# Optimization experiments

Hardware: AMD Instinct MI355X
Metric: run time of the kernel (lower is better)

The kernel has to match this reference:

```python
import jax, jax.numpy as jnp
import numpy as np

LN_EPS = 1e-5

def layer_norm(x, w, b):
    mu = jnp.mean(x, axis=-1, keepdims=True)
    var = jnp.mean(jnp.square(x - mu), axis=-1, keepdims=True)
    return (x - mu) * jax.lax.rsqrt(var + LN_EPS) * w + b

def adaptive_mask_np(aa, bb, ada_para=0.2):
    # True = disallowed (matches torch ~bool mask). Static shapes -> numpy.
    adaptive_num = int(bb * ada_para)
    cc = bb // aa
    i = np.arange(aa)
    start = i * cc
    end = start + cc + adaptive_num
    over = end > bb - 1
    start = np.where(over, np.maximum(start - (end - (bb - 1)), 0), start)
    end = np.where(over, bb, end)
    cols = np.arange(bb)
    allowed = (cols[None, :] >= start[:, None]) & (cols[None, :] < end[:, None])
    return jnp.asarray(~allowed)  # [aa, bb] bool

def setup_inputs() -> dict:
    key = jax.random.key(0)
    ks = jax.random.split(key, 20)
    Lq, Lk, B, d, dff = 512, 4096, 4, 512, 2048
    s = lambda k, shape: jax.random.normal(k, shape, dtype=jnp.float32) * 0.02
    inp = {
        'tgt': jax.random.normal(ks[0], (Lq, B, d), dtype=jnp.float32),
        'memory': jax.random.normal(ks[1], (Lk, B, d), dtype=jnp.float32),
        'Wq': s(ks[2], (d, d)), 'bq': jnp.zeros((d,), jnp.float32),
        'Wk': s(ks[3], (d, d)), 'bk': jnp.zeros((d,), jnp.float32),
        'Wv': s(ks[4], (d, d)), 'bv': jnp.zeros((d,), jnp.float32),
        'Wo': s(ks[5], (d, d)), 'bo': jnp.zeros((d,), jnp.float32),
        'W1': s(ks[6], (dff, d)), 'b1': jnp.zeros((dff,), jnp.float32),
        'W2': s(ks[7], (d, dff)), 'b2': jnp.zeros((d,), jnp.float32),
        'ln1_w': jnp.ones((d,), jnp.float32), 'ln1_b': jnp.zeros((d,), jnp.float32),
        'ln2_w': jnp.ones((d,), jnp.float32), 'ln2_b': jnp.zeros((d,), jnp.float32),
        'ln3_w': jnp.ones((d,), jnp.float32), 'ln3_b': jnp.zeros((d,), jnp.float32),
        'ln4_w': jnp.ones((d,), jnp.float32), 'ln4_b': jnp.zeros((d,), jnp.float32),
    }
    return inp

def reference(tgt, memory, Wq, bq, Wk, bk, Wv, bv, Wo, bo, W1, b1, W2, b2,
              ln1_w, ln1_b, ln2_w, ln2_b, ln3_w, ln3_b, ln4_w, ln4_b):
    Lq, B, d = tgt.shape
    Lk = memory.shape[0]
    H = 8
    hd = d // H
    scale = 1.0 / jnp.sqrt(jnp.asarray(hd, tgt.dtype))

    t = layer_norm(tgt, ln1_w, ln1_b)      # [Lq,B,d]
    m = layer_norm(memory, ln2_w, ln2_b)   # [Lk,B,d]

    mask = adaptive_mask_np(Lq, Lk, 0.2)   # [Lq,Lk] bool, True=masked

    q = (t @ Wq.T + bq).reshape(Lq, B, H, hd)
    k = (m @ Wk.T + bk).reshape(Lk, B, H, hd)
    v = (m @ Wv.T + bv).reshape(Lk, B, H, hd)

    scores = jnp.einsum('qbhd,kbhd->bhqk', q * scale, k)
    scores = jnp.where(mask[None, None], -jnp.inf, scores)
    p = jax.nn.softmax(scores, axis=-1)                   # [B,H,Lq,Lk]
    attn_weights = jnp.mean(p, axis=1)                    # [B,Lq,Lk] (avg over heads)

    ctx = jnp.einsum('bhqk,kbhd->qbhd', p, v).reshape(Lq, B, d)
    tgt2 = ctx @ Wo.T + bo

    x = t + tgt2                       # dropout1 = identity (eval)
    x = layer_norm(x, ln3_w, ln3_b)
    ff = jax.nn.relu(x @ W1.T + b1) @ W2.T + b2
    x = x + ff                         # dropout2 = identity (eval)
    x = layer_norm(x, ln4_w, ln4_b)
    return (x, attn_weights)
```

## Files before the change

### kernel.cpp

```cpp
#include <hip/hip_runtime.h>
#include <hip/hip_bf16.h>

typedef __hip_bfloat16 bf16_t;
typedef __bf16 bf16x8 __attribute__((ext_vector_type(8)));
typedef float f32x4 __attribute__((ext_vector_type(4)));

#define LQ 512
#define LK 4096
#define BATCH 4
#define DMODEL 512
#define NHEAD 8
#define HEADDIM 64
#define DFF 2048
#define LN_EPS 1e-5f

__device__ inline float tofl(float x) { return x; }
__device__ inline float tofl(bf16_t x) { return __bfloat162float(x); }
__device__ inline void stfl(float* p, float v) { *p = v; }
__device__ inline void stfl(bf16_t* p, float v) { *p = __float2bfloat16(v); }

__device__ __forceinline__ void gld_lds16(const bf16_t* g, void* lds_base) {
    __builtin_amdgcn_global_load_lds(
        (const __attribute__((address_space(1))) uint32_t*)g,
        (__attribute__((address_space(3))) uint32_t*)lds_base, 16, 0, 0);
}

__global__ void prep_kernel(const float* __restrict__ s0, const float* __restrict__ s1,
                            const float* __restrict__ s2, const float* __restrict__ s3,
                            const float* __restrict__ s4, const float* __restrict__ s5,
                            bf16_t* __restrict__ wqkvo, bf16_t* __restrict__ w1bf,
                            bf16_t* __restrict__ w2bf, float* __restrict__ zbuf) {
    int bid = blockIdx.x;
    int tid = threadIdx.x;
    if (bid < 3072) {
        int t = bid * 256 + tid;
        int which = t >> 16;
        int idx = (t & 65535) * 4;
        const float* s; bf16_t* d;
        if (which < 4) {
            s = (which == 0 ? s0 : which == 1 ? s1 : which == 2 ? s2 : s3) ;
            d = wqkvo + (size_t)which * 262144;
        } else if (which < 8) {
            s = s4 + (size_t)(which - 4) * 262144;
            d = w1bf + (size_t)(which - 4) * 262144;
        } else {
            s = s5 + (size_t)(which - 8) * 262144;
            d = w2bf + (size_t)(which - 8) * 262144;
        }
        float4 v = *(const float4*)(s + idx);
        d[idx + 0] = __float2bfloat16(v.x);
        d[idx + 1] = __float2bfloat16(v.y);
        d[idx + 2] = __float2bfloat16(v.z);
        d[idx + 3] = __float2bfloat16(v.w);
    } else {
        size_t i = ((size_t)(bid - 3072) * 256 + tid) * 4;
        float4 z = {0.f, 0.f, 0.f, 0.f};
        *(float4*)(zbuf + i) = z;
    }
}

template <typename TOUT, bool DUAL>
__global__ void ln_kernel(const float* __restrict__ in, const float* __restrict__ w,
                          const float* __restrict__ b, TOUT* __restrict__ out1,
                          float* __restrict__ out2) {
    __shared__ float red[256];
    const int row = blockIdx.x;
    const int tid = threadIdx.x;
    const float* x = in + (size_t)row * DMODEL;
    float v0 = x[tid];
    float v1 = x[tid + 256];

    red[tid] = v0 + v1;
    __syncthreads();
    for (int s = 128; s > 0; s >>= 1) { if (tid < s) red[tid] += red[tid + s]; __syncthreads(); }
    float mu = red[0] * (1.0f / DMODEL);
    __syncthreads();

    float d0 = v0 - mu, d1 = v1 - mu;
    red[tid] = d0 * d0 + d1 * d1;
    __syncthreads();
    for (int s = 128; s > 0; s >>= 1) { if (tid < s) red[tid] += red[tid + s]; __syncthreads(); }
    float inv = rsqrtf(red[0] * (1.0f / DMODEL) + LN_EPS);

    float r0 = d0 * inv * w[tid] + b[tid];
    float r1 = d1 * inv * w[tid + 256] + b[tid + 256];
    TOUT* o = out1 + (size_t)row * DMODEL;
    stfl(&o[tid], r0);
    stfl(&o[tid + 256], r1);
    if (DUAL) {
        float* o2 = out2 + (size_t)row * DMODEL;
        o2[tid] = r0;
        o2[tid + 256] = r1;
    }
}

__global__ void ln12_kernel(const float* __restrict__ tgt, const float* __restrict__ memory,
                            const float* __restrict__ w1, const float* __restrict__ b1,
                            const float* __restrict__ w2, const float* __restrict__ b2,
                            bf16_t* __restrict__ t_bf, float* __restrict__ t_f32,
                            bf16_t* __restrict__ m_buf) {
    __shared__ float red[256];
    const int row = blockIdx.x;
    const int tid = threadIdx.x;
    const float* in; const float* w; const float* b;
    bf16_t* o1; float* o2; bool dual;
    if (row < 2048) {
        in = tgt + (size_t)row * DMODEL; w = w1; b = b1;
        o1 = t_bf + (size_t)row * DMODEL; o2 = t_f32 + (size_t)row * DMODEL; dual = true;
    } else {
        int r2 = row - 2048;
        in = memory + (size_t)r2 * DMODEL; w = w2; b = b2;
        o1 = m_buf + (size_t)r2 * DMODEL; o2 = nullptr; dual = false;
    }
    float v0 = in[tid];
    float v1 = in[tid + 256];
    red[tid] = v0 + v1;
    __syncthreads();
    for (int s = 128; s > 0; s >>= 1) { if (tid < s) red[tid] += red[tid + s]; __syncthreads(); }
    float mu = red[0] * (1.0f / DMODEL);
    __syncthreads();
    float d0 = v0 - mu, d1 = v1 - mu;
    red[tid] = d0 * d0 + d1 * d1;
    __syncthreads();
    for (int s = 128; s > 0; s >>= 1) { if (tid < s) red[tid] += red[tid + s]; __syncthreads(); }
    float inv = rsqrtf(red[0] * (1.0f / DMODEL) + LN_EPS);
    float r0 = d0 * inv * w[tid] + b[tid];
    float r1 = d1 * inv * w[tid + 256] + b[tid + 256];
    o1[tid] = __float2bfloat16(r0);
    o1[tid + 256] = __float2bfloat16(r1);
    if (dual) {
        o2[tid] = r0;
        o2[tid + 256] = r1;
    }
}

template <int TN, typename TC, bool RELU, bool RESID>
__global__ __launch_bounds__(256) void gemm_mfma(
        const bf16_t* __restrict__ A, const bf16_t* __restrict__ B,
        const float* __restrict__ bias, const float* __restrict__ resid,
        TC* __restrict__ C, int M, int N, int K) {
    __shared__ uint4 As4[1024];
    __shared__ uint4 Bs4[TN * 8];

    const int tid = threadIdx.x;
    const int lane = tid & 63;
    const int wave = tid >> 6;
    const int row16 = lane & 15;
    const int quad = lane >> 4;
    const int n0 = blockIdx.x * TN;
    const int m0 = blockIdx.y * 128;

    constexpr int MI = (TN == 128) ? 4 : 2;
    const int wy = (TN == 128) ? (wave >> 1) : wave;
    const int wx = (TN == 128) ? (wave & 1) : 0;
    const int m_base = wy * ((TN == 128) ? 64 : 32);
    const int n_base = wx * 64;

    const int rr = lane >> 3;
    const int kc = (lane & 7) ^ rr;
    const int kx = row16 & 7;

    const bf16_t* AsE = (const bf16_t*)As4;
    const bf16_t* BsE = (const bf16_t*)Bs4;

    f32x4 acc[MI][4] = {};

    for (int k0 = 0; k0 < K; k0 += 64) {
#pragma unroll
        for (int it = 0; it < 4; it++) {
            int issue = it * 4 + wave;
            int r = issue * 8 + rr;
            gld_lds16(A + (size_t)(m0 + r) * K + k0 + kc * 8, &As4[issue * 64]);
        }
#pragma unroll
        for (int it = 0; it < TN / 32; it++) {
            int issue = it * 4 + wave;
            int r = issue * 8 + rr;
            gld_lds16(B + (size_t)(n0 + r) * K + k0 + kc * 8, &Bs4[issue * 64]);
        }
        __syncthreads();
#pragma unroll
        for (int s = 0; s < 2; s++) {
            const int kq = s * 4 + quad;
            const int kcs = (kq ^ kx) * 8;
            bf16x8 af[MI], bfr[4];
#pragma unroll
            for (int i = 0; i < MI; i++)
                af[i] = *(const bf16x8*)&AsE[(m_base + i * 16 + row16) * 64 + kcs];
#pragma unroll
            for (int j = 0; j < 4; j++)
                bfr[j] = *(const bf16x8*)&BsE[(n_base + j * 16 + row16) * 64 + kcs];
#pragma unroll
            for (int i = 0; i < MI; i++)
#pragma unroll
                for (int j = 0; j < 4; j++)
                    acc[i][j] = __builtin_amdgcn_mfma_f32_16x16x32_bf16(af[i], bfr[j], acc[i][j], 0, 0, 0);
        }
        __syncthreads();
    }

#pragma unroll
    for (int i = 0; i < MI; i++) {
#pragma unroll
        for (int j = 0; j < 4; j++) {
            int col = n0 + n_base + j * 16 + row16;
            float bsv = bias[col];
#pragma unroll
            for (int r = 0; r < 4; r++) {
                int row = m0 + m_base + i * 16 + quad * 4 + r;
                float val = acc[i][j][r] + bsv;
                if (RESID) val += resid[(size_t)row * N + col];
                if (RELU) val = fmaxf(val, 0.0f);
                stfl(&C[(size_t)row * N + col], val);
            }
        }
    }
}

__global__ __launch_bounds__(256) void transpose_kv(const bf16_t* __restrict__ kb,
                                                    bf16_t* __restrict__ kT) {
    __shared__ bf16_t tile[64][80];
    const int kt = blockIdx.x * 64;
    const int ct = blockIdx.y * 64;
    const int b  = blockIdx.z;
    const int t = threadIdx.x;
    {
        int kl = t >> 2, cl = (t & 3) * 16;
        const bf16_t* src = kb + ((size_t)(kt + kl) * 4 + b) * 512 + ct + cl;
        *(uint4*)&tile[kl][cl]     = *(const uint4*)src;
        *(uint4*)&tile[kl][cl + 8] = *(const uint4*)(src + 8);
    }
    __syncthreads();
    {
        int cl2 = t >> 2, ks = (t & 3) * 16;
        __attribute__((aligned(16))) bf16_t vals[16];
#pragma unroll
        for (int j = 0; j < 16; j++) vals[j] = tile[ks + j][cl2];
        bf16_t* dst = kT + ((size_t)b * 512 + ct + cl2) * 4096 + kt + ks;
        *(uint4*)dst       = *(const uint4*)&vals[0];
        *(uint4*)(dst + 8) = *(const uint4*)&vals[8];
    }
}

__global__ __launch_bounds__(256, 2) void attn_mfma(
        const bf16_t* __restrict__ qb,
        const bf16_t* __restrict__ kb,
        const bf16_t* __restrict__ vT,
        bf16_t* __restrict__ ctx,
        float* __restrict__ attn_out) {
    const int d = blockIdx.x;
    const int g = d & 7;
    const int b = g >> 1;
    const int qhalf = g & 1;
    const int i_in = d >> 3;
    const int hg = i_in & 1;
    const int qt = qhalf * 32 + (i_in >> 1);
    const int q0 = qt * 8;
    const int tid = threadIdx.x;
    const int lane = tid & 63;
    const int w = tid >> 6;
    const int h = hg * 4 + w;
    const int hoffg = h * HEADDIM;
    const int hl = w * HEADDIM;
    const int row16 = lane & 15;
    const int quad = lane >> 4;

    __align__(16) __shared__ bf16_t Qs[8][264];
    __align__(16) __shared__ bf16_t Zrow[904];
    __align__(16) __shared__ bf16_t Ps[4][8][904];
    __shared__ float Ls[4][8];

    int us; { int s = q0 * 8, e = s + 827; if (e > 4095) s = 3268; us = s; }
    int sq[4], eq[4];
#pragma unroll
    for (int r = 0; r < 4; r++) {
        int ql = quad * 4 + r;
        if (ql < 8) {
            int s = (q0 + ql) * 8, e = s + 827;
            if (e > 4095) { s = 3268; e = 4096; }
            sq[r] = s; eq[r] = e;
        } else { sq[r] = 0; eq[r] = 0; }
    }

    {
        int r = tid >> 5, coff = (tid & 31) * 8;
        *(uint4*)&Qs[r][coff] =
            *(const uint4*)(qb + ((size_t)(q0 + r) * 4 + b) * 512 + hg * 256 + coff);
        if (tid < 113) { uint4 z = {0, 0, 0, 0}; *(uint4*)&Zrow[tid * 8] = z; }
    }
    __syncthreads();

    const bf16_t* q0p = (row16 < 8) ? &Qs[row16][hl + quad * 8] : &Zrow[0];
    const bf16_t* q1p = (row16 < 8) ? &Qs[row16][hl + 32 + quad * 8] : &Zrow[8];
    const bf16x8 aq0 = *(const bf16x8*)q0p;
    const bf16x8 aq1 = *(const bf16x8*)q1p;

    float l[4] = {0.f, 0.f, 0.f, 0.f};
    for (int c = 0; c < 7; c++) {
        const int cb = c * 128;
#pragma unroll
        for (int t8 = 0; t8 < 8; t8++) {
            int key = us + cb + t8 * 16 + row16;
            int key_eff = key > 4095 ? 4095 : key;
            const bf16_t* kr = kb + (size_t)key_eff * 2048 + (size_t)b * 512 + hoffg;
            bf16x8 bk0 = *(const bf16x8*)(kr + quad * 8);
            bf16x8 bk1 = *(const bf16x8*)(kr + 32 + quad * 8);
            f32x4 acc = {};
            acc = __builtin_amdgcn_mfma_f32_16x16x32_bf16(aq0, bk0, acc, 0, 0, 0);
            acc = __builtin_amdgcn_mfma_f32_16x16x32_bf16(aq1, bk1, acc, 0, 0, 0);
#pragma unroll
            for (int r = 0; r < 4; r++) {
                int ql = quad * 4 + r;
                bool valid = (key >= sq[r]) && (key < eq[r]);
                float p = valid ? __expf(0.125f * acc[r]) : 0.0f;
                l[r] += p;
                if (ql < 8) Ps[w][ql][cb + t8 * 16 + row16] = __float2bfloat16(p);
            }
        }
    }
#pragma unroll
    for (int off = 1; off < 16; off <<= 1) {
#pragma unroll
        for (int r = 0; r < 4; r++) l[r] += __shfl_xor(l[r], off, 64);
    }
    float linv[4];
#pragma unroll
    for (int r = 0; r < 4; r++) linv[r] = 1.0f / l[r];
    if (row16 == 0) {
#pragma unroll
        for (int r = 0; r < 4; r++) {
            int ql = quad * 4 + r;
            if (ql < 8) Ls[w][ql] = linv[r];
        }
    }
    __syncthreads();

    {
        int qq = tid >> 5;
        int ln2 = tid & 31;
        float ls0 = Ls[0][qq] * 0.125f, ls1 = Ls[1][qq] * 0.125f;
        float ls2 = Ls[2][qq] * 0.125f, ls3 = Ls[3][qq] * 0.125f;
        float* base = attn_out + ((size_t)b * LQ + q0 + qq) * LK + us;
        const int cmax = LK - us;
        for (int col = ln2; col < 896; col += 32) {
            if (col < cmax) {
                float s = ls0 * tofl(Ps[0][qq][col]) + ls1 * tofl(Ps[1][qq][col]) +
                          ls2 * tofl(Ps[2][qq][col]) + ls3 * tofl(Ps[3][qq][col]);
                atomicAdd(base + col, s);
            }
        }
    }

    f32x4 o[4] = {};
    for (int c = 0; c < 7; c++) {
        const int cb = c * 128;
#pragma unroll
        for (int kt2 = 0; kt2 < 4; kt2++) {
            const bf16_t* ap_src = (row16 < 8) ? &Ps[w][row16][cb + kt2 * 32 + quad * 8]
                                               : &Zrow[0];
            bf16x8 ap = *(const bf16x8*)ap_src;
#pragma unroll
            for (int nt = 0; nt < 4; nt++) {
                const bf16_t* vr = vT + ((size_t)b * 512 + hoffg + nt * 16 + row16) * 4096
                                   + us + cb + kt2 * 32 + quad * 8;
                bf16x8 bv = *(const bf16x8*)vr;
                o[nt] = __builtin_amdgcn_mfma_f32_16x16x32_bf16(ap, bv, o[nt], 0, 0, 0);
            }
        }
    }
#pragma unroll
    for (int nt = 0; nt < 4; nt++) {
#pragma unroll
        for (int r = 0; r < 4; r++) {
            int ql = quad * 4 + r;
            if (ql < 8) {
                ctx[((size_t)(q0 + ql) * 4 + b) * 512 + hoffg + nt * 16 + row16] =
                    __float2bfloat16(o[nt][r] * linv[r]);
            }
        }
    }
}

extern "C" void kernel_launch(void* const* d_in, const int* in_sizes, int n_in,
                              void* d_out, int out_size, void* d_ws, size_t ws_size,
                              hipStream_t stream) {
    const float* tgt    = (const float*)d_in[0];
    const float* memory = (const float*)d_in[1];
    const float* Wq = (const float*)d_in[2];
    const float* bq = (const float*)d_in[3];
    const float* Wk = (const float*)d_in[4];
    const float* bk = (const float*)d_in[5];
    const float* Wv = (const float*)d_in[6];
    const float* bv = (const float*)d_in[7];
    const float* Wo = (const float*)d_in[8];
    const float* bo = (const float*)d_in[9];
    const float* W1 = (const float*)d_in[10];
    const float* b1 = (const float*)d_in[11];
    const float* W2 = (const float*)d_in[12];
    const float* b2 = (const float*)d_in[13];
    const float* ln1w = (const float*)d_in[14];
    const float* ln1b = (const float*)d_in[15];
    const float* ln2w = (const float*)d_in[16];
    const float* ln2b = (const float*)d_in[17];
    const float* ln3w = (const float*)d_in[18];
    const float* ln3b = (const float*)d_in[19];
    const float* ln4w = (const float*)d_in[20];
    const float* ln4b = (const float*)d_in[21];

    const size_t M1 = (size_t)LQ * BATCH;
    const size_t M2 = (size_t)LK * BATCH;
    const size_t SZ1 = M1 * DMODEL;

    char* wsb = (char*)d_ws;
    const size_t MB = 1 << 20;
    bf16_t* m_buf   = (bf16_t*)(wsb + 0 * MB);
    bf16_t* vT_buf  = (bf16_t*)(wsb + 0 * MB);
    bf16_t* h_buf   = (bf16_t*)(wsb + 0 * MB);
    float*  xln_f   = (float*)(wsb + 8 * MB);
    float*  x2_buf  = (float*)(wsb + 12 * MB);
    bf16_t* k_buf   = (bf16_t*)(wsb + 16 * MB);
    bf16_t* v_buf   = (bf16_t*)(wsb + 32 * MB);
    float*  xres    = (float*)(wsb + 32 * MB);
    bf16_t* t_bf    = (bf16_t*)(wsb + 48 * MB);
    bf16_t* xln_bf  = (bf16_t*)(wsb + 48 * MB);
    float*  t_f32   = (float*)(wsb + 50 * MB);
    bf16_t* q_bf    = (bf16_t*)(wsb + 54 * MB);
    bf16_t* W2_bf   = (bf16_t*)(wsb + 56 * MB);
    bf16_t* ctx_buf = (bf16_t*)(wsb + 58 * MB);
    bf16_t* wqkvo   = (bf16_t*)(wsb + 60 * MB);
    bf16_t* W1_bf   = (bf16_t*)(wsb + 62 * MB);

    bf16_t* Wq_bf = wqkvo;
    bf16_t* Wk_bf = wqkvo + 262144;
    bf16_t* Wv_bf = wqkvo + 2 * 262144;
    bf16_t* Wo_bf = wqkvo + 3 * 262144;

    float* out_x    = (float*)d_out;
    float* out_attn = out_x + SZ1;

    prep_kernel<<<dim3(11264), dim3(256), 0, stream>>>(
        Wq, Wk, Wv, Wo, W1, W2, wqkvo, W1_bf, W2_bf, out_attn);

    ln12_kernel<<<dim3(M1 + M2), dim3(256), 0, stream>>>(
        tgt, memory, ln1w, ln1b, ln2w, ln2b, t_bf, t_f32, m_buf);

    gemm_mfma<64, bf16_t, false, false><<<dim3(8, 16), dim3(256), 0, stream>>>(
        t_bf, Wq_bf, bq, nullptr, q_bf, M1, DMODEL, DMODEL);
    gemm_mfma<128, bf16_t, false, false><<<dim3(4, 128), dim3(256), 0, stream>>>(
        m_buf, Wk_bf, bk, nullptr, k_buf, M2, DMODEL, DMODEL);
    gemm_mfma<128, bf16_t, false, false><<<dim3(4, 128), dim3(256), 0, stream>>>(
        m_buf, Wv_bf, bv, nullptr, v_buf, M2, DMODEL, DMODEL);

    transpose_kv<<<dim3(64, 8, 4), dim3(256), 0, stream>>>(v_buf, vT_buf);

    attn_mfma<<<dim3(512), dim3(256), 0, stream>>>(q_bf, k_buf, vT_buf, ctx_buf, out_attn);

    gemm_mfma<64, float, false, true><<<dim3(8, 16), dim3(256), 0, stream>>>(
        ctx_buf, Wo_bf, bo, t_f32, xres, M1, DMODEL, DMODEL);

    ln_kernel<bf16_t, true><<<dim3(M1), dim3(256), 0, stream>>>(xres, ln3w, ln3b, xln_bf, xln_f);

    gemm_mfma<128, bf16_t, true, false><<<dim3(16, 16), dim3(256), 0, stream>>>(
        xln_bf, W1_bf, b1, nullptr, h_buf, M1, DFF, DMODEL);

    gemm_mfma<64, float, false, true><<<dim3(8, 16), dim3(256), 0, stream>>>(
        h_buf, W2_bf, b2, xln_f, x2_buf, M1, DMODEL, DFF);

    ln_kernel<float, false><<<dim3(M1), dim3(256), 0, stream>>>(x2_buf, ln4w, ln4b, out_x, nullptr);
}
```

Before: 332.8 us.

## Split attention key range across two wave halves per block with LDS reduction

Doubles the attention block to 512 threads so each head is handled by two waves, each covering half of the key window for both QK/softmax and PV. Partial row sums and partial PV outputs are combined through shared memory, and the Ps buffer is reused to hold the output partials. The aim is more parallelism and latency hiding in the attention stage, which previously launched only 512 blocks of 4 waves. The cost is extra barriers, an LDS reduction, and higher register pressure under the new launch bounds.

```diff
diff --git a/kernel.cpp b/kernel.cpp
--- a/kernel.cpp
+++ b/kernel.cpp
@@ -242,7 +242,7 @@
     }
 }
 
-__global__ __launch_bounds__(256, 2) void attn_mfma(
+__global__ __launch_bounds__(512, 4) void attn_mfma(
         const bf16_t* __restrict__ qb,
         const bf16_t* __restrict__ kb,
         const bf16_t* __restrict__ vT,
@@ -258,17 +258,19 @@
     const int q0 = qt * 8;
     const int tid = threadIdx.x;
     const int lane = tid & 63;
-    const int w = tid >> 6;
-    const int h = hg * 4 + w;
+    const int w8 = tid >> 6;
+    const int hw = w8 & 3;
+    const int half = w8 >> 2;
+    const int h = hg * 4 + hw;
     const int hoffg = h * HEADDIM;
-    const int hl = w * HEADDIM;
+    const int hl = hw * HEADDIM;
     const int row16 = lane & 15;
     const int quad = lane >> 4;
 
     __align__(16) __shared__ bf16_t Qs[8][264];
     __align__(16) __shared__ bf16_t Zrow[904];
     __align__(16) __shared__ bf16_t Ps[4][8][904];
-    __shared__ float Ls[4][8];
+    __shared__ float Ls2[2][4][8];
 
     int us; { int s = q0 * 8, e = s + 827; if (e > 4095) s = 3268; us = s; }
     int sq[4], eq[4];
@@ -282,7 +284,7 @@
         } else { sq[r] = 0; eq[r] = 0; }
     }
 
-    {
+    if (tid < 256) {
         int r = tid >> 5, coff = (tid & 31) * 8;
         *(uint4*)&Qs[r][coff] =
             *(const uint4*)(qb + ((size_t)(q0 + r) * 4 + b) * 512 + hg * 256 + coff);
@@ -296,53 +298,59 @@
     const bf16x8 aq1 = *(const bf16x8*)q1p;
 
     float l[4] = {0.f, 0.f, 0.f, 0.f};
-    for (int c = 0; c < 7; c++) {
+    const int it0 = half * 28;
+#pragma unroll 4
+    for (int it = it0; it < it0 + 28; ++it) {
+        const int c = it >> 3;
+        const int t8 = it & 7;
         const int cb = c * 128;
-#pragma unroll
-        for (int t8 = 0; t8 < 8; t8++) {
-            int key = us + cb + t8 * 16 + row16;
-            int key_eff = key > 4095 ? 4095 : key;
-            const bf16_t* kr = kb + (size_t)key_eff * 2048 + (size_t)b * 512 + hoffg;
-            bf16x8 bk0 = *(const bf16x8*)(kr + quad * 8);
-            bf16x8 bk1 = *(const bf16x8*)(kr + 32 + quad * 8);
-            f32x4 acc = {};
-            acc = __builtin_amdgcn_mfma_f32_16x16x32_bf16(aq0, bk0, acc, 0, 0, 0);
-            acc = __builtin_amdgcn_mfma_f32_16x16x32_bf16(aq1, bk1, acc, 0, 0, 0);
-#pragma unroll
-            for (int r = 0; r < 4; r++) {
-                int ql = quad * 4 + r;
-                bool valid = (key >= sq[r]) && (key < eq[r]);
-                float p = valid ? __expf(0.125f * acc[r]) : 0.0f;
-                l[r] += p;
-                if (ql < 8) Ps[w][ql][cb + t8 * 16 + row16] = __float2bfloat16(p);
-            }
-        }
-    }
-#pragma unroll
-    for (int off = 1; off < 16; off <<= 1) {
-#pragma unroll
-        for (int r = 0; r < 4; r++) l[r] += __shfl_xor(l[r], off, 64);
-    }
-    float linv[4];
-#pragma unroll
-    for (int r = 0; r < 4; r++) linv[r] = 1.0f / l[r];
-    if (row16 == 0) {
+        int key = us + cb + t8 * 16 + row16;
+        int key_eff = key > 4095 ? 4095 : key;
+        const bf16_t* kr = kb + (size_t)key_eff * 2048 + (size_t)b * 512 + hoffg;
+        bf16x8 bk0 = *(const bf16x8*)(kr + quad * 8);
+        bf16x8 bk1 = *(const bf16x8*)(kr + 32 + quad * 8);
+        f32x4 acc = {};
+        acc = __builtin_amdgcn_mfma_f32_16x16x32_bf16(aq0, bk0, acc, 0, 0, 0);
+        acc = __builtin_amdgcn_mfma_f32_16x16x32_bf16(aq1, bk1, acc, 0, 0, 0);
 #pragma unroll
         for (int r = 0; r < 4; r++) {
             int ql = quad * 4 + r;
-            if (ql < 8) Ls[w][ql] = linv[r];
-        }
-    }
-    __syncthreads();
+            bool valid = (key >= sq[r]) && (key < eq[r]);
+            float p = valid ? __expf(0.125f * acc[r]) : 0.0f;
+            l[r] += p;
+            if (ql < 8) Ps[hw][ql][cb + t8 * 16 + row16] = __float2bfloat16(p);
+        }
+    }
+#pragma unroll
+    for (int off = 1; off < 16; off <<= 1) {
+#pragma unroll
+        for (int r = 0; r < 4; r++) l[r] += __shfl_xor(l[r], off, 64);
+    }
+    if (row16 == 0) {
+#pragma unroll
+        for (int r = 0; r < 4; r++) {
+            int ql = quad * 4 + r;
+            if (ql < 8) Ls2[half][hw][ql] = l[r];
+        }
+    }
+    __syncthreads();
+
+    float linv[4];
+#pragma unroll
+    for (int r = 0; r < 4; r++) {
+        int ql = quad * 4 + r;
+        linv[r] = (ql < 8) ? 1.0f / (Ls2[0][hw][ql] + Ls2[1][hw][ql]) : 0.0f;
+    }
 
     {
-        int qq = tid >> 5;
-        int ln2 = tid & 31;
-        float ls0 = Ls[0][qq] * 0.125f, ls1 = Ls[1][qq] * 0.125f;
-        float ls2 = Ls[2][qq] * 0.125f, ls3 = Ls[3][qq] * 0.125f;
+        int qq = w8;
+        float ls0 = 0.125f / (Ls2[0][0][qq] + Ls2[1][0][qq]);
+        float ls1 = 0.125f / (Ls2[0][1][qq] + Ls2[1][1][qq]);
+        float ls2 = 0.125f / (Ls2[0][2][qq] + Ls2[1][2][qq]);
+        float ls3 = 0.125f / (Ls2[0][3][qq] + Ls2[1][3][qq]);
         float* base = attn_out + ((size_t)b * LQ + q0 + qq) * LK + us;
         const int cmax = LK - us;
-        for (int col = ln2; col < 896; col += 32) {
+        for (int col = lane; col < 896; col += 64) {
             if (col < cmax) {
                 float s = ls0 * tofl(Ps[0][qq][col]) + ls1 * tofl(Ps[1][qq][col]) +
                           ls2 * tofl(Ps[2][qq][col]) + ls3 * tofl(Ps[3][qq][col]);
@@ -352,30 +360,48 @@
     }
 
     f32x4 o[4] = {};
-    for (int c = 0; c < 7; c++) {
+    const int pv0 = half * 14;
+#pragma unroll 2
+    for (int it = pv0; it < pv0 + 14; ++it) {
+        const int c = it >> 2;
+        const int kt2 = it & 3;
         const int cb = c * 128;
-#pragma unroll
-        for (int kt2 = 0; kt2 < 4; kt2++) {
-            const bf16_t* ap_src = (row16 < 8) ? &Ps[w][row16][cb + kt2 * 32 + quad * 8]
-                                               : &Zrow[0];
-            bf16x8 ap = *(const bf16x8*)ap_src;
-#pragma unroll
-            for (int nt = 0; nt < 4; nt++) {
-                const bf16_t* vr = vT + ((size_t)b * 512 + hoffg + nt * 16 + row16) * 4096
-                                   + us + cb + kt2 * 32 + quad * 8;
-                bf16x8 bv = *(const bf16x8*)vr;
-                o[nt] = __builtin_amdgcn_mfma_f32_16x16x32_bf16(ap, bv, o[nt], 0, 0, 0);
+        const bf16_t* ap_src = (row16 < 8) ? &Ps[hw][row16][cb + kt2 * 32 + quad * 8]
+                                           : &Zrow[0];
+        bf16x8 ap = *(const bf16x8*)ap_src;
+#pragma unroll
+        for (int nt = 0; nt < 4; nt++) {
+            const bf16_t* vr = vT + ((size_t)b * 512 + hoffg + nt * 16 + row16) * 4096
+                               + us + cb + kt2 * 32 + quad * 8;
+            bf16x8 bv = *(const bf16x8*)vr;
+            o[nt] = __builtin_amdgcn_mfma_f32_16x16x32_bf16(ap, bv, o[nt], 0, 0, 0);
+        }
+    }
+
+    __syncthreads();
+    float* Osum = (float*)Ps;
+    if (half == 1) {
+#pragma unroll
+        for (int nt = 0; nt < 4; nt++) {
+#pragma unroll
+            for (int r = 0; r < 4; r++) {
+                int ql = quad * 4 + r;
+                if (ql < 8) Osum[(hw * 8 + ql) * 65 + nt * 16 + row16] = o[nt][r];
             }
         }
     }
-#pragma unroll
-    for (int nt = 0; nt < 4; nt++) {
-#pragma unroll
-        for (int r = 0; r < 4; r++) {
-            int ql = quad * 4 + r;
-            if (ql < 8) {
-                ctx[((size_t)(q0 + ql) * 4 + b) * 512 + hoffg + nt * 16 + row16] =
-                    __float2bfloat16(o[nt][r] * linv[r]);
+    __syncthreads();
+    if (half == 0) {
+#pragma unroll
+        for (int nt = 0; nt < 4; nt++) {
+#pragma unroll
+            for (int r = 0; r < 4; r++) {
+                int ql = quad * 4 + r;
+                if (ql < 8) {
+                    float tot = o[nt][r] + Osum[(hw * 8 + ql) * 65 + nt * 16 + row16];
+                    ctx[((size_t)(q0 + ql) * 4 + b) * 512 + hoffg + nt * 16 + row16] =
+                        __float2bfloat16(tot * linv[r]);
+                }
             }
         }
     }
@@ -453,7 +479,7 @@
 
     transpose_kv<<<dim3(64, 8, 4), dim3(256), 0, stream>>>(v_buf, vT_buf);
 
-    attn_mfma<<<dim3(512), dim3(256), 0, stream>>>(q_bf, k_buf, vT_buf, ctx_buf, out_attn);
+    attn_mfma<<<dim3(512), dim3(512), 0, stream>>>(q_bf, k_buf, vT_buf, ctx_buf, out_attn);
 
     gemm_mfma<64, float, false, true><<<dim3(8, 16), dim3(256), 0, stream>>>(
         ctx_buf, Wo_bf, bo, t_f32, xres, M1, DMODEL, DMODEL);
```

Measured after the change: 331.1 us. No clear change (-0.5%).

## Process all eight heads per attention block and drop atomic head-average

Applied to the files above, without the earlier changes.

The attention kernel now uses 512 threads, one wave per head, so each block covers all eight heads for a query tile. The head-averaged attention weights can then be written directly instead of accumulated with atomicAdd across two blocks. K and V^T buffers are padded (row strides 2064/4112) to avoid cache or channel conflicts, which needs a remapped store in the K GEMM. W2 conversion moves to a separate kernel to fit the new workspace layout. The cost is a large dynamic LDS footprint (~126KB), leaving one block per CU, and only 256 blocks in the grid.

```diff
diff --git a/kernel.cpp b/kernel.cpp
--- a/kernel.cpp
+++ b/kernel.cpp
@@ -14,6 +14,9 @@
 #define DFF 2048
 #define LN_EPS 1e-5f
 
+#define KSTR 2064
+#define VSTR 4112
+
 __device__ inline float tofl(float x) { return x; }
 __device__ inline float tofl(bf16_t x) { return __bfloat162float(x); }
 __device__ inline void stfl(float* p, float v) { *p = v; }
@@ -27,25 +30,22 @@
 
 __global__ void prep_kernel(const float* __restrict__ s0, const float* __restrict__ s1,
                             const float* __restrict__ s2, const float* __restrict__ s3,
-                            const float* __restrict__ s4, const float* __restrict__ s5,
+                            const float* __restrict__ s4,
                             bf16_t* __restrict__ wqkvo, bf16_t* __restrict__ w1bf,
-                            bf16_t* __restrict__ w2bf, float* __restrict__ zbuf) {
+                            float* __restrict__ zbuf) {
     int bid = blockIdx.x;
     int tid = threadIdx.x;
-    if (bid < 3072) {
+    if (bid < 2048) {
         int t = bid * 256 + tid;
         int which = t >> 16;
         int idx = (t & 65535) * 4;
         const float* s; bf16_t* d;
         if (which < 4) {
-            s = (which == 0 ? s0 : which == 1 ? s1 : which == 2 ? s2 : s3) ;
+            s = (which == 0 ? s0 : which == 1 ? s1 : which == 2 ? s2 : s3);
             d = wqkvo + (size_t)which * 262144;
-        } else if (which < 8) {
+        } else {
             s = s4 + (size_t)(which - 4) * 262144;
             d = w1bf + (size_t)(which - 4) * 262144;
-        } else {
-            s = s5 + (size_t)(which - 8) * 262144;
-            d = w2bf + (size_t)(which - 8) * 262144;
         }
         float4 v = *(const float4*)(s + idx);
         d[idx + 0] = __float2bfloat16(v.x);
@@ -53,10 +53,19 @@
         d[idx + 2] = __float2bfloat16(v.z);
         d[idx + 3] = __float2bfloat16(v.w);
     } else {
-        size_t i = ((size_t)(bid - 3072) * 256 + tid) * 4;
+        size_t i = ((size_t)(bid - 2048) * 256 + tid) * 4;
         float4 z = {0.f, 0.f, 0.f, 0.f};
         *(float4*)(zbuf + i) = z;
     }
+}
+
+__global__ void conv_w2(const float* __restrict__ s, bf16_t* __restrict__ d) {
+    int i = (blockIdx.x * 256 + threadIdx.x) * 4;
+    float4 v = *(const float4*)(s + i);
+    d[i + 0] = __float2bfloat16(v.x);
+    d[i + 1] = __float2bfloat16(v.y);
+    d[i + 2] = __float2bfloat16(v.z);
+    d[i + 3] = __float2bfloat16(v.w);
 }
 
 template <typename TOUT, bool DUAL>
@@ -134,7 +143,7 @@
     }
 }
 
-template <int TN, typename TC, bool RELU, bool RESID>
+template <int TN, typename TC, bool RELU, bool RESID, bool KREMAP = false>
 __global__ __launch_bounds__(256) void gemm_mfma(
         const bf16_t* __restrict__ A, const bf16_t* __restrict__ B,
         const float* __restrict__ bias, const float* __restrict__ resid,
@@ -211,7 +220,10 @@
                 float val = acc[i][j][r] + bsv;
                 if (RESID) val += resid[(size_t)row * N + col];
                 if (RELU) val = fmaxf(val, 0.0f);
-                stfl(&C[(size_t)row * N + col], val);
+                size_t caddr = KREMAP
+                    ? ((size_t)(row >> 2) * KSTR + (size_t)(row & 3) * 512 + col)
+                    : ((size_t)row * N + col);
+                stfl(&C[caddr], val);
             }
         }
     }
@@ -236,39 +248,33 @@
         __attribute__((aligned(16))) bf16_t vals[16];
 #pragma unroll
         for (int j = 0; j < 16; j++) vals[j] = tile[ks + j][cl2];
-        bf16_t* dst = kT + ((size_t)b * 512 + ct + cl2) * 4096 + kt + ks;
+        bf16_t* dst = kT + ((size_t)b * 512 + ct + cl2) * VSTR + kt + ks;
         *(uint4*)dst       = *(const uint4*)&vals[0];
         *(uint4*)(dst + 8) = *(const uint4*)&vals[8];
     }
 }
 
-__global__ __launch_bounds__(256, 2) void attn_mfma(
+__global__ __launch_bounds__(512, 1) void attn_mfma(
         const bf16_t* __restrict__ qb,
         const bf16_t* __restrict__ kb,
         const bf16_t* __restrict__ vT,
         bf16_t* __restrict__ ctx,
         float* __restrict__ attn_out) {
-    const int d = blockIdx.x;
-    const int g = d & 7;
-    const int b = g >> 1;
-    const int qhalf = g & 1;
-    const int i_in = d >> 3;
-    const int hg = i_in & 1;
-    const int qt = qhalf * 32 + (i_in >> 1);
+    extern __shared__ char smem[];
+    bf16_t* Ps   = (bf16_t*)smem;
+    bf16_t* Qs   = (bf16_t*)(smem + 115712);
+    bf16_t* Zrow = (bf16_t*)(smem + 115712 + 8320);
+    float*  Ls   = (float*)(smem + 115712 + 8320 + 1808);
+
+    const int b  = blockIdx.x & 3;
+    const int qt = blockIdx.x >> 2;
     const int q0 = qt * 8;
     const int tid = threadIdx.x;
     const int lane = tid & 63;
-    const int w = tid >> 6;
-    const int h = hg * 4 + w;
+    const int h = tid >> 6;
     const int hoffg = h * HEADDIM;
-    const int hl = w * HEADDIM;
     const int row16 = lane & 15;
     const int quad = lane >> 4;
-
-    __align__(16) __shared__ bf16_t Qs[8][264];
-    __align__(16) __shared__ bf16_t Zrow[904];
-    __align__(16) __shared__ bf16_t Ps[4][8][904];
-    __shared__ float Ls[4][8];
 
     int us; { int s = q0 * 8, e = s + 827; if (e > 4095) s = 3268; us = s; }
     int sq[4], eq[4];
@@ -283,39 +289,36 @@
     }
 
     {
-        int r = tid >> 5, coff = (tid & 31) * 8;
-        *(uint4*)&Qs[r][coff] =
-            *(const uint4*)(qb + ((size_t)(q0 + r) * 4 + b) * 512 + hg * 256 + coff);
+        int r = tid >> 6, coff = (tid & 63) * 8;
+        *(uint4*)&Qs[r * 520 + coff] =
+            *(const uint4*)(qb + ((size_t)(q0 + r) * 4 + b) * 512 + coff);
         if (tid < 113) { uint4 z = {0, 0, 0, 0}; *(uint4*)&Zrow[tid * 8] = z; }
     }
     __syncthreads();
 
-    const bf16_t* q0p = (row16 < 8) ? &Qs[row16][hl + quad * 8] : &Zrow[0];
-    const bf16_t* q1p = (row16 < 8) ? &Qs[row16][hl + 32 + quad * 8] : &Zrow[8];
+    const bf16_t* q0p = (row16 < 8) ? &Qs[row16 * 520 + hoffg + quad * 8] : &Zrow[0];
+    const bf16_t* q1p = (row16 < 8) ? &Qs[row16 * 520 + hoffg + 32 + quad * 8] : &Zrow[8];
     const bf16x8 aq0 = *(const bf16x8*)q0p;
     const bf16x8 aq1 = *(const bf16x8*)q1p;
 
     float l[4] = {0.f, 0.f, 0.f, 0.f};
-    for (int c = 0; c < 7; c++) {
-        const int cb = c * 128;
-#pragma unroll
-        for (int t8 = 0; t8 < 8; t8++) {
-            int key = us + cb + t8 * 16 + row16;
-            int key_eff = key > 4095 ? 4095 : key;
-            const bf16_t* kr = kb + (size_t)key_eff * 2048 + (size_t)b * 512 + hoffg;
-            bf16x8 bk0 = *(const bf16x8*)(kr + quad * 8);
-            bf16x8 bk1 = *(const bf16x8*)(kr + 32 + quad * 8);
-            f32x4 acc = {};
-            acc = __builtin_amdgcn_mfma_f32_16x16x32_bf16(aq0, bk0, acc, 0, 0, 0);
-            acc = __builtin_amdgcn_mfma_f32_16x16x32_bf16(aq1, bk1, acc, 0, 0, 0);
-#pragma unroll
-            for (int r = 0; r < 4; r++) {
-                int ql = quad * 4 + r;
-                bool valid = (key >= sq[r]) && (key < eq[r]);
-                float p = valid ? __expf(0.125f * acc[r]) : 0.0f;
-                l[r] += p;
-                if (ql < 8) Ps[w][ql][cb + t8 * 16 + row16] = __float2bfloat16(p);
-            }
+#pragma unroll 4
+    for (int it = 0; it < 56; ++it) {
+        int key = us + it * 16 + row16;
+        int key_eff = key > 4095 ? 4095 : key;
+        const bf16_t* kr = kb + (size_t)key_eff * KSTR + b * 512 + hoffg;
+        bf16x8 bk0 = *(const bf16x8*)(kr + quad * 8);
+        bf16x8 bk1 = *(const bf16x8*)(kr + 32 + quad * 8);
+        f32x4 acc = {};
+        acc = __builtin_amdgcn_mfma_f32_16x16x32_bf16(aq0, bk0, acc, 0, 0, 0);
+        acc = __builtin_amdgcn_mfma_f32_16x16x32_bf16(aq1, bk1, acc, 0, 0, 0);
+#pragma unroll
+        for (int r = 0; r < 4; r++) {
+            int ql = quad * 4 + r;
+            bool valid = (key >= sq[r]) && (key < eq[r]);
+            float p = valid ? __expf(0.125f * acc[r]) : 0.0f;
+            l[r] += p;
+            if (ql < 8) Ps[(h * 8 + ql) * 904 + it * 16 + row16] = __float2bfloat16(p);
         }
     }
 #pragma unroll
@@ -330,44 +333,43 @@
 #pragma unroll
         for (int r = 0; r < 4; r++) {
             int ql = quad * 4 + r;
-            if (ql < 8) Ls[w][ql] = linv[r];
-        }
-    }
-    __syncthreads();
+            if (ql < 8) Ls[h * 8 + ql] = linv[r];
+        }
+    }
+    __syncthreads();
+
+    f32x4 o[4] = {};
+#pragma unroll 2
+    for (int it = 0; it < 28; ++it) {
+        const bf16_t* ap_src = (row16 < 8) ? &Ps[(h * 8 + row16) * 904 + it * 32 + quad * 8]
+                                           : &Zrow[0];
+        bf16x8 ap = *(const bf16x8*)ap_src;
+#pragma unroll
+        for (int nt = 0; nt < 4; ++nt) {
+            const bf16_t* vr = vT + ((size_t)(b * 512 + hoffg + nt * 16 + row16)) * VSTR
+                               + us + it * 32 + quad * 8;
+            bf16x8 bv = *(const bf16x8*)vr;
+            o[nt] = __builtin_amdgcn_mfma_f32_16x16x32_bf16(ap, bv, o[nt], 0, 0, 0);
+        }
+    }
 
     {
-        int qq = tid >> 5;
-        int ln2 = tid & 31;
-        float ls0 = Ls[0][qq] * 0.125f, ls1 = Ls[1][qq] * 0.125f;
-        float ls2 = Ls[2][qq] * 0.125f, ls3 = Ls[3][qq] * 0.125f;
+        int qq = h;
+        float ls[8];
+#pragma unroll
+        for (int hh = 0; hh < 8; ++hh) ls[hh] = 0.125f * Ls[hh * 8 + qq];
         float* base = attn_out + ((size_t)b * LQ + q0 + qq) * LK + us;
         const int cmax = LK - us;
-        for (int col = ln2; col < 896; col += 32) {
+        for (int col = lane; col < 896; col += 64) {
             if (col < cmax) {
-                float s = ls0 * tofl(Ps[0][qq][col]) + ls1 * tofl(Ps[1][qq][col]) +
-                          ls2 * tofl(Ps[2][qq][col]) + ls3 * tofl(Ps[3][qq][col]);
-                atomicAdd(base + col, s);
+                float s = 0.f;
+#pragma unroll
+                for (int hh = 0; hh < 8; ++hh) s += ls[hh] * tofl(Ps[(hh * 8 + qq) * 904 + col]);
+                base[col] = s;
             }
         }
     }
 
-    f32x4 o[4] = {};
-    for (int c = 0; c < 7; c++) {
-        const int cb = c * 128;
-#pragma unroll
-        for (int kt2 = 0; kt2 < 4; kt2++) {
-            const bf16_t* ap_src = (row16 < 8) ? &Ps[w][row16][cb + kt2 * 32 + quad * 8]
-                                               : &Zrow[0];
-            bf16x8 ap = *(const bf16x8*)ap_src;
-#pragma unroll
-            for (int nt = 0; nt < 4; nt++) {
-                const bf16_t* vr = vT + ((size_t)b * 512 + hoffg + nt * 16 + row16) * 4096
-                                   + us + cb + kt2 * 32 + quad * 8;
-                bf16x8 bv = *(const bf16x8*)vr;
-                o[nt] = __builtin_amdgcn_mfma_f32_16x16x32_bf16(ap, bv, o[nt], 0, 0, 0);
-            }
-        }
-    }
 #pragma unroll
     for (int nt = 0; nt < 4; nt++) {
 #pragma unroll
@@ -416,16 +418,16 @@
     bf16_t* m_buf   = (bf16_t*)(wsb + 0 * MB);
     bf16_t* vT_buf  = (bf16_t*)(wsb + 0 * MB);
     bf16_t* h_buf   = (bf16_t*)(wsb + 0 * MB);
-    float*  xln_f   = (float*)(wsb + 8 * MB);
-    float*  x2_buf  = (float*)(wsb + 12 * MB);
-    bf16_t* k_buf   = (bf16_t*)(wsb + 16 * MB);
-    bf16_t* v_buf   = (bf16_t*)(wsb + 32 * MB);
-    float*  xres    = (float*)(wsb + 32 * MB);
-    bf16_t* t_bf    = (bf16_t*)(wsb + 48 * MB);
-    bf16_t* xln_bf  = (bf16_t*)(wsb + 48 * MB);
-    float*  t_f32   = (float*)(wsb + 50 * MB);
-    bf16_t* q_bf    = (bf16_t*)(wsb + 54 * MB);
-    bf16_t* W2_bf   = (bf16_t*)(wsb + 56 * MB);
+    bf16_t* k_buf   = (bf16_t*)(wsb + 17 * MB);
+    float*  xres    = (float*)(wsb + 17 * MB);
+    float*  xln_f   = (float*)(wsb + 21 * MB);
+    float*  x2_buf  = (float*)(wsb + 25 * MB);
+    bf16_t* W2_bf   = (bf16_t*)(wsb + 34 * MB);
+    bf16_t* v_buf   = (bf16_t*)(wsb + 34 * MB);
+    bf16_t* t_bf    = (bf16_t*)(wsb + 50 * MB);
+    bf16_t* xln_bf  = (bf16_t*)(wsb + 50 * MB);
+    float*  t_f32   = (float*)(wsb + 52 * MB);
+    bf16_t* q_bf    = (bf16_t*)(wsb + 56 * MB);
     bf16_t* ctx_buf = (bf16_t*)(wsb + 58 * MB);
     bf16_t* wqkvo   = (bf16_t*)(wsb + 60 * MB);
     bf16_t* W1_bf   = (bf16_t*)(wsb + 62 * MB);
@@ -438,22 +440,28 @@
     float* out_x    = (float*)d_out;
     float* out_attn = out_x + SZ1;
 
-    prep_kernel<<<dim3(11264), dim3(256), 0, stream>>>(
-        Wq, Wk, Wv, Wo, W1, W2, wqkvo, W1_bf, W2_bf, out_attn);
+    prep_kernel<<<dim3(10240), dim3(256), 0, stream>>>(
+        Wq, Wk, Wv, Wo, W1, wqkvo, W1_bf, out_attn);
 
     ln12_kernel<<<dim3(M1 + M2), dim3(256), 0, stream>>>(
         tgt, memory, ln1w, ln1b, ln2w, ln2b, t_bf, t_f32, m_buf);
 
     gemm_mfma<64, bf16_t, false, false><<<dim3(8, 16), dim3(256), 0, stream>>>(
         t_bf, Wq_bf, bq, nullptr, q_bf, M1, DMODEL, DMODEL);
-    gemm_mfma<128, bf16_t, false, false><<<dim3(4, 128), dim3(256), 0, stream>>>(
+    gemm_mfma<128, bf16_t, false, false, true><<<dim3(4, 128), dim3(256), 0, stream>>>(
         m_buf, Wk_bf, bk, nullptr, k_buf, M2, DMODEL, DMODEL);
     gemm_mfma<128, bf16_t, false, false><<<dim3(4, 128), dim3(256), 0, stream>>>(
         m_buf, Wv_bf, bv, nullptr, v_buf, M2, DMODEL, DMODEL);
 
     transpose_kv<<<dim3(64, 8, 4), dim3(256), 0, stream>>>(v_buf, vT_buf);
 
-    attn_mfma<<<dim3(512), dim3(256), 0, stream>>>(q_bf, k_buf, vT_buf, ctx_buf, out_attn);
+    conv_w2<<<dim3(1024), dim3(256), 0, stream>>>(W2, W2_bf);
+
+    const int attn_lds = 115712 + 8320 + 1808 + 256;
+    hipFuncSetAttribute((const void*)attn_mfma,
+                        hipFuncAttributeMaxDynamicSharedMemorySize, attn_lds);
+    attn_mfma<<<dim3(256), dim3(512), attn_lds, stream>>>(
+        q_bf, k_buf, vT_buf, ctx_buf, out_attn);
 
     gemm_mfma<64, float, false, true><<<dim3(8, 16), dim3(256), 0, stream>>>(
         ctx_buf, Wo_bf, bo, t_f32, xres, M1, DMODEL, DMODEL);
```

After: 325.1 us. 2.3% less time.
